# Optimization experiments

Hardware: AMD Instinct MI355X
Metric: run time of the kernel (lower is better)

Reference implementation:

```python
import jax, jax.numpy as jnp
import numpy as np

B, H, W, IMG_CH = 64, 16, 16, 1024
N, TEXT_CH = 256, 768
FQ = FK = 512


def _glorot(key, shape, fan_in, fan_out):
    lim = np.sqrt(6.0 / (fan_in + fan_out)).astype(np.float32)
    return jax.random.uniform(key, shape, jnp.float32, -lim, lim)


def setup_inputs() -> dict:
    key = jax.random.key(0)
    ks = jax.random.split(key, 8)
    x1 = jax.random.normal(ks[0], (B, H, W, IMG_CH), jnp.float32)
    x2 = jax.random.normal(ks[1], (B, N, TEXT_CH), jnp.float32)
    # padding mask over text tokens, broadcast over image pixels
    masks = (jax.random.uniform(ks[2], (B, N, 1)) > 0.1).astype(jnp.float32)
    kernel_q = _glorot(ks[3], (1, 1, IMG_CH, FQ), IMG_CH, FQ)
    kernel_k = _glorot(ks[4], (1, TEXT_CH, FK), TEXT_CH, FK)
    kernel_v = _glorot(ks[5], (1, TEXT_CH, IMG_CH), TEXT_CH, IMG_CH)
    kernel_o = _glorot(ks[6], (1, 1, IMG_CH, IMG_CH), IMG_CH, IMG_CH)
    return {
        "x1": x1, "x2": x2, "masks": masks,
        "kernel_q": kernel_q, "bias_q": jnp.zeros((FQ,), jnp.float32),
        "kernel_k": kernel_k, "bias_k": jnp.zeros((FK,), jnp.float32),
        "kernel_v": kernel_v, "bias_v": jnp.zeros((IMG_CH,), jnp.float32),
        "kernel_o": kernel_o, "bias_o": jnp.zeros((IMG_CH,), jnp.float32),
    }


def reference(x1, x2, masks, kernel_q, bias_q, kernel_k, bias_k,
              kernel_v, bias_v, kernel_o, bias_o):
    b, h, w, c = x1.shape
    # 1x1 conv2d == pointwise matmul over channels
    q = jnp.einsum('bhwc,cf->bhwf', x1, kernel_q[0, 0]) + bias_q   # (B,H,W,512)
    # width-1 conv1d == pointwise matmul over channels
    k = jnp.einsum('bnc,cf->bnf', x2, kernel_k[0]) + bias_k        # (B,N,512)
    v = jnp.einsum('bnc,cf->bnf', x2, kernel_v[0]) + bias_v        # (B,N,IMG_CH)
    qf = q.reshape(b, h * w, -1)                                   # (B,HW,512)
    s = jnp.einsum('bqd,bnd->bqn', qf, k)                          # (B,HW,N)
    beta = jax.nn.softmax(s, axis=-1)
    # NON-STANDARD: mask applied AFTER softmax (no renormalization)
    beta = beta * jnp.swapaxes(masks, 1, 2)                        # (B,HW,N)*(B,1,N)
    o = jnp.einsum('bqn,bnf->bqf', beta, v).reshape(b, h, w, c)    # (B,H,W,IMG_CH)
    o = jnp.einsum('bhwc,cf->bhwf', o, kernel_o[0, 0]) + bias_o
    return o, beta
```

## Files before the change

### kernel.cpp

```cpp
#include <hip/hip_runtime.h>
#include <hip/hip_bf16.h>

using bf16 = __hip_bfloat16;

typedef __attribute__((ext_vector_type(8))) short short8;
typedef __attribute__((ext_vector_type(4))) short shortx4;
typedef __attribute__((ext_vector_type(4))) float f32x4;

#define MFMA_BF16(a, b, c) __builtin_amdgcn_mfma_f32_16x16x32_bf16((a), (b), (c), 0, 0, 0)

__device__ __forceinline__ void lds_load16(const void* g, void* l) {
    __builtin_amdgcn_global_load_lds(
        (const __attribute__((address_space(1))) void*)g,
        (__attribute__((address_space(3))) void*)l, 16, 0, 0);
}

__device__ __forceinline__ void swiz_xcd(int& bx, int& by) {
    const int NX = gridDim.x, NY = gridDim.y;
    const int flat = blockIdx.y * NX + blockIdx.x;
    const int cid = flat & 7, slot = flat >> 3;
    by = cid * (NY >> 3) + slot / NX;
    bx = slot % NX;
}

__device__ __forceinline__ void stage_async_128(const bf16* src, int ld, bf16* tile,
                                                int wave, int lane) {
    const int r = lane >> 2, c = (lane & 3) * 8;
#pragma unroll
    for (int p = 0; p < 2; ++p) {
        const int row = p * 64 + wave * 16;
        lds_load16(src + (size_t)(row + r) * ld + c, tile + row * 32);
    }
}
__device__ __forceinline__ void stage_async_256_w8(const bf16* src, int ld, bf16* tile,
                                                   int wave, int lane) {
    const int r = lane >> 2, c = (lane & 3) * 8;
#pragma unroll
    for (int p = 0; p < 2; ++p) {
        const int row = p * 128 + wave * 16;
        lds_load16(src + (size_t)(row + r) * ld + c, tile + row * 32);
    }
}
template <bool SPLIT>
__device__ __forceinline__ void stage_conv_128(const float* src, int ld, bf16* th,
                                               bf16* tl, int tid) {
#pragma unroll
    for (int it = 0; it < 4; ++it) {
        const int vid = tid + 256 * it;
        const int row = vid >> 3, col = (vid & 7) * 4;
        const f32x4 x = *(const f32x4*)(src + (size_t)row * ld + col);
        shortx4 h, l;
#pragma unroll
        for (int j = 0; j < 4; ++j) {
            bf16 hb = __float2bfloat16(x[j]);
            h[j] = *(short*)&hb;
            if constexpr (SPLIT) {
                bf16 lb = __float2bfloat16(x[j] - __bfloat162float(hb));
                l[j] = *(short*)&lb;
            }
        }
        *(shortx4*)(&th[row * 40 + col]) = h;
        if constexpr (SPLIT) *(shortx4*)(&tl[row * 40 + col]) = l;
    }
}

template <bool SPLIT>
__global__ void transpose_split(const float* __restrict__ in, bf16* __restrict__ outh,
                                bf16* __restrict__ outl, int K, int N) {
    __shared__ float t[32][33];
    const int n0 = blockIdx.x * 32, k0 = blockIdx.y * 32;
    const int tx = threadIdx.x, ty = threadIdx.y;
#pragma unroll
    for (int i = 0; i < 4; ++i)
        t[ty + i * 8][tx] = in[(size_t)(k0 + ty + i * 8) * N + n0 + tx];
    __syncthreads();
#pragma unroll
    for (int i = 0; i < 4; ++i) {
        const float x = t[tx][ty + i * 8];
        const bf16 hb = __float2bfloat16(x);
        const size_t idx = (size_t)(n0 + ty + i * 8) * K + k0 + tx;
        outh[idx] = hb;
        if constexpr (SPLIT) outl[idx] = __float2bfloat16(x - __bfloat162float(hb));
    }
}

enum { G_SPLIT3 = 0, G_VT = 1, G_F32 = 2, G_PV = 3 };

template <int MODE>
__global__ __launch_bounds__(256) void gemm2(
    const void* __restrict__ Av, const bf16* __restrict__ Bth,
    const bf16* __restrict__ Btl, const float* __restrict__ bias,
    void* __restrict__ out0, void* __restrict__ out1, int N, int K) {
    constexpr bool ASPLIT = (MODE == G_SPLIT3);
    constexpr bool ACONV = (MODE == G_SPLIT3 || MODE == G_VT);
    constexpr int LDA = ACONV ? 40 : 32;
    constexpr int SZ_A = 128 * LDA * 2;
    constexpr int SZ_AL = ASPLIT ? 128 * 40 * 2 : 0;
    constexpr int SZ_B = 128 * 32 * 2;
    constexpr int STAGE = SZ_A + SZ_AL + SZ_B + (ASPLIT ? SZ_B : 0);
    constexpr int SMEM =
        (MODE == G_VT) ? (STAGE > 128 * 136 * 2 ? STAGE : 128 * 136 * 2) : STAGE;
    __shared__ __align__(16) char smem[SMEM];
    bf16* AsH = (bf16*)smem;
    bf16* AsL = (bf16*)(smem + SZ_A);
    bf16* BsH = (bf16*)(smem + SZ_A + SZ_AL);
    bf16* BsL = (bf16*)(smem + SZ_A + SZ_AL + SZ_B);
    bf16* Ts = (bf16*)smem;

    const int tid = threadIdx.x, wave = tid >> 6, lane = tid & 63;
    const int quad = lane >> 4, l15 = lane & 15;
    const int wr = wave >> 1, wc = wave & 1;

    int bx, by;
    if constexpr (MODE == G_PV) {
        bx = blockIdx.x;
        by = blockIdx.y;
    } else {
        swiz_xcd(bx, by);
    }
    const int m0 = by * 128, n0 = bx * 128;
    const int z = blockIdx.z;

    const float* Af = (const float*)Av;
    const bf16* Ab = (const bf16*)Av;
    const bf16* Bh = Bth;
    if constexpr (MODE == G_PV) {
        Ab += (size_t)z * 256 * 256;
        Bh += (size_t)z * 1024 * 256;
    }

    f32x4 acc[4][4] = {};
    for (int k0 = 0; k0 < K; k0 += 32) {
        if constexpr (ACONV)
            stage_conv_128<ASPLIT>(Af + (size_t)m0 * K + k0, K, AsH, AsL, tid);
        else
            stage_async_128(Ab + (size_t)m0 * K + k0, K, AsH, wave, lane);
        stage_async_128(Bh + (size_t)n0 * K + k0, K, BsH, wave, lane);
        if constexpr (ASPLIT)
            stage_async_128(Btl + (size_t)n0 * K + k0, K, BsL, wave, lane);
        __syncthreads();

        short8 ah[4], bh[4];
#pragma unroll
        for (int t = 0; t < 4; ++t) {
            ah[t] = *(const short8*)(&AsH[(wr * 64 + t * 16 + l15) * LDA + quad * 8]);
            bh[t] = *(const short8*)(&BsH[(wc * 64 + t * 16 + l15) * 32 + quad * 8]);
        }
        if constexpr (ASPLIT) {
            short8 al[4], bl[4];
#pragma unroll
            for (int t = 0; t < 4; ++t) {
                al[t] = *(const short8*)(&AsL[(wr * 64 + t * 16 + l15) * 40 + quad * 8]);
                bl[t] = *(const short8*)(&BsL[(wc * 64 + t * 16 + l15) * 32 + quad * 8]);
            }
#pragma unroll
            for (int ti = 0; ti < 4; ++ti)
#pragma unroll
                for (int tj = 0; tj < 4; ++tj) {
                    acc[ti][tj] = MFMA_BF16(al[ti], bh[tj], acc[ti][tj]);
                    acc[ti][tj] = MFMA_BF16(ah[ti], bl[tj], acc[ti][tj]);
                    acc[ti][tj] = MFMA_BF16(ah[ti], bh[tj], acc[ti][tj]);
                }
        } else {
#pragma unroll
            for (int ti = 0; ti < 4; ++ti)
#pragma unroll
                for (int tj = 0; tj < 4; ++tj)
                    acc[ti][tj] = MFMA_BF16(ah[ti], bh[tj], acc[ti][tj]);
        }
        __syncthreads();
    }

    float bv4[4] = {0.f, 0.f, 0.f, 0.f};
    if constexpr (MODE != G_PV) {
#pragma unroll
        for (int tj = 0; tj < 4; ++tj) bv4[tj] = bias[n0 + wc * 64 + tj * 16 + l15];
    }

    if constexpr (MODE == G_VT) {
#pragma unroll
        for (int ti = 0; ti < 4; ++ti)
#pragma unroll
            for (int tj = 0; tj < 4; ++tj)
#pragma unroll
                for (int i = 0; i < 4; ++i) {
                    const int ml = wr * 64 + ti * 16 + quad * 4 + i;
                    const int nl = wc * 64 + tj * 16 + l15;
                    Ts[nl * 136 + ml] = __float2bfloat16(acc[ti][tj][i] + bv4[tj]);
                }
        __syncthreads();
        const int bIdx = m0 >> 8, tok0 = m0 & 255;
        const int nl = tid >> 1, half = tid & 1;
        bf16* dst = (bf16*)out0 + ((size_t)bIdx * N + n0 + nl) * 256 + tok0 + half * 64;
        const bf16* src = &Ts[nl * 136 + half * 64];
#pragma unroll
        for (int j = 0; j < 8; ++j)
            *(short8*)(dst + j * 8) = *(const short8*)(src + j * 8);
    } else {
#pragma unroll
        for (int ti = 0; ti < 4; ++ti)
#pragma unroll
            for (int tj = 0; tj < 4; ++tj)
#pragma unroll
                for (int i = 0; i < 4; ++i) {
                    const size_t row = m0 + wr * 64 + ti * 16 + quad * 4 + i;
                    const size_t col = n0 + wc * 64 + tj * 16 + l15;
                    const float v = acc[ti][tj][i] + bv4[tj];
                    if constexpr (MODE == G_F32) {
                        ((float*)out0)[row * N + col] = v;
                    } else if constexpr (MODE == G_PV) {
                        ((bf16*)out0)[((size_t)z * 256 + row) * N + col] =
                            __float2bfloat16(v);
                    } else {
                        const bf16 hb = __float2bfloat16(v);
                        ((bf16*)out0)[row * N + col] = hb;
                        ((bf16*)out1)[row * N + col] =
                            __float2bfloat16(v - __bfloat162float(hb));
                    }
                }
    }
}

__global__ __launch_bounds__(512) void attn_s(
    const bf16* __restrict__ qh, const bf16* __restrict__ ql,
    const bf16* __restrict__ kh, const bf16* __restrict__ kl,
    const float* __restrict__ masks, float* __restrict__ beta_out,
    bf16* __restrict__ betaB) {
    __shared__ bf16 kH[256 * 32], kL[256 * 32];
    __shared__ float redM[4][32], redS[4][32];
    int qt, b;
    swiz_xcd(qt, b);
    const int tid = threadIdx.x, wave = tid >> 6, lane = tid & 63;
    const int quad = lane >> 4, l15 = lane & 15;
    const int wr = wave >> 2, wq = wave & 3;

    f32x4 acc[4] = {};
    const size_t qoff = ((size_t)(b * 256 + qt * 32 + wr * 16 + l15)) * 512;
    const size_t kbase = (size_t)(b * 256) * 512;

    for (int k0 = 0; k0 < 512; k0 += 32) {
        stage_async_256_w8(kh + kbase + k0, 512, kH, wave, lane);
        stage_async_256_w8(kl + kbase + k0, 512, kL, wave, lane);
        __syncthreads();
        const short8 aH = *(const short8*)(qh + qoff + k0 + quad * 8);
        const short8 aL = *(const short8*)(ql + qoff + k0 + quad * 8);
#pragma unroll
        for (int nt = 0; nt < 4; ++nt) {
            const int kr = wq * 64 + nt * 16 + l15;
            const short8 bH = *(const short8*)(&kH[kr * 32 + quad * 8]);
            const short8 bL = *(const short8*)(&kL[kr * 32 + quad * 8]);
            acc[nt] = MFMA_BF16(aH, bH, acc[nt]);
            acc[nt] = MFMA_BF16(aH, bL, acc[nt]);
            acc[nt] = MFMA_BF16(aL, bH, acc[nt]);
        }
        __syncthreads();
    }

    float pm[4], ps[4];
#pragma unroll
    for (int i = 0; i < 4; ++i) {
        float m = fmaxf(fmaxf(acc[0][i], acc[1][i]), fmaxf(acc[2][i], acc[3][i]));
#pragma unroll
        for (int s = 1; s < 16; s <<= 1) m = fmaxf(m, __shfl_xor(m, s));
        float sum = 0.f;
#pragma unroll
        for (int nt = 0; nt < 4; ++nt) sum += __expf(acc[nt][i] - m);
#pragma unroll
        for (int s = 1; s < 16; s <<= 1) sum += __shfl_xor(sum, s);
        pm[i] = m;
        ps[i] = sum;
    }
    if (l15 == 0) {
#pragma unroll
        for (int i = 0; i < 4; ++i) {
            redM[wq][wr * 16 + quad * 4 + i] = pm[i];
            redS[wq][wr * 16 + quad * 4 + i] = ps[i];
        }
    }
    __syncthreads();
    float gm[4], ginv[4];
#pragma unroll
    for (int i = 0; i < 4; ++i) {
        const int r = wr * 16 + quad * 4 + i;
        const float m = fmaxf(fmaxf(redM[0][r], redM[1][r]), fmaxf(redM[2][r], redM[3][r]));
        const float s = redS[0][r] * __expf(redM[0][r] - m) +
                        redS[1][r] * __expf(redM[1][r] - m) +
                        redS[2][r] * __expf(redM[2][r] - m) +
                        redS[3][r] * __expf(redM[3][r] - m);
        gm[i] = m;
        ginv[i] = 1.0f / s;
    }
#pragma unroll
    for (int nt = 0; nt < 4; ++nt) {
        const int col = wq * 64 + nt * 16 + l15;
        const float mv = masks[b * 256 + col];
#pragma unroll
        for (int i = 0; i < 4; ++i) {
            const int row = qt * 32 + wr * 16 + quad * 4 + i;
            const float bvv = __expf(acc[nt][i] - gm[i]) * ginv[i] * mv;
            const size_t idx = ((size_t)(b * 256 + row)) * 256 + col;
            beta_out[idx] = bvv;
            betaB[idx] = __float2bfloat16(bvv);
        }
    }
}

extern "C" void kernel_launch(void* const* d_in, const int* in_sizes, int n_in,
                              void* d_out, int out_size, void* d_ws, size_t ws_size,
                              hipStream_t stream) {
    const float* x1 = (const float*)d_in[0];
    const float* x2 = (const float*)d_in[1];
    const float* masks = (const float*)d_in[2];
    const float* Wq = (const float*)d_in[3];
    const float* bq = (const float*)d_in[4];
    const float* Wk = (const float*)d_in[5];
    const float* bk = (const float*)d_in[6];
    const float* Wv = (const float*)d_in[7];
    const float* bv = (const float*)d_in[8];
    const float* Wo = (const float*)d_in[9];
    const float* bo = (const float*)d_in[10];

    char* ws = (char*)d_ws;
    bf16* WqTh = (bf16*)(ws + 0);
    bf16* WqTl = (bf16*)(ws + 1048576);
    bf16* WkTh = (bf16*)(ws + 2097152);
    bf16* WkTl = (bf16*)(ws + 2883584);
    bf16* WvTh = (bf16*)(ws + 3670016);
    bf16* WoTh = (bf16*)(ws + 5242880);
    bf16* qh = (bf16*)(ws + 7340032);
    bf16* ql = (bf16*)(ws + 24117248);
    bf16* kh = (bf16*)(ws + 40894464);
    bf16* kl = (bf16*)(ws + 57671680);
    bf16* vT = (bf16*)(ws + 74448896);
    bf16* betaB = (bf16*)(ws + 108003328);
    bf16* o_mid = (bf16*)(ws + 7340032);

    float* out_o = (float*)d_out;
    float* out_beta = out_o + (size_t)16384 * 1024;

    const dim3 tb(32, 8);
    transpose_split<true><<<dim3(16, 32), tb, 0, stream>>>(Wq, WqTh, WqTl, 1024, 512);
    transpose_split<true><<<dim3(16, 24), tb, 0, stream>>>(Wk, WkTh, WkTl, 768, 512);
    transpose_split<false><<<dim3(32, 24), tb, 0, stream>>>(Wv, WvTh, nullptr, 768, 1024);
    transpose_split<false><<<dim3(32, 32), tb, 0, stream>>>(Wo, WoTh, nullptr, 1024, 1024);

    gemm2<G_SPLIT3><<<dim3(4, 128), 256, 0, stream>>>(x1, WqTh, WqTl, bq, qh, ql, 512, 1024);
    gemm2<G_SPLIT3><<<dim3(4, 128), 256, 0, stream>>>(x2, WkTh, WkTl, bk, kh, kl, 512, 768);
    gemm2<G_VT><<<dim3(8, 128), 256, 0, stream>>>(x2, WvTh, nullptr, bv, vT, nullptr, 1024, 768);

    attn_s<<<dim3(8, 64), 512, 0, stream>>>(qh, ql, kh, kl, masks, out_beta, betaB);

    gemm2<G_PV><<<dim3(8, 2, 64), 256, 0, stream>>>(betaB, vT, nullptr, nullptr, o_mid,
                                                    nullptr, 1024, 256);
    gemm2<G_F32><<<dim3(8, 128), 256, 0, stream>>>(o_mid, WoTh, nullptr, bo, out_o,
                                                   nullptr, 1024, 1024);
}
```

Measured before the change: 472.3 us.

## Stage fp32 A tiles via async LDS loads and XOR-swizzle LDS tiles

The A operand of the converting GEMMs is no longer loaded into registers, split into bf16 hi/lo and written to padded LDS. It is now copied raw as fp32 into LDS with async global_load_lds, and the bf16 hi/lo split happens at fragment-read time. All bf16 and fp32 LDS tiles also get an XOR swizzle on the 16-byte column chunk to avoid bank conflicts without padding. This removes the synchronous conversion stage and its register round trip. In exchange, each wave repeats the conversion for the fragments it reads, and the fp32 A tile takes more LDS.

```diff
diff --git a/kernel.cpp b/kernel.cpp
--- a/kernel.cpp
+++ b/kernel.cpp
@@ -23,44 +23,56 @@
     bx = slot % NX;
 }
 
-__device__ __forceinline__ void stage_async_128(const bf16* src, int ld, bf16* tile,
-                                                int wave, int lane) {
-    const int r = lane >> 2, c = (lane & 3) * 8;
+__device__ __forceinline__ void stage_bf16_128(const bf16* src, int ld, bf16* tile,
+                                               int wave, int lane) {
+    const int r = lane >> 2;
+    const int c = ((lane & 3) ^ ((r >> 1) & 3)) * 8;
 #pragma unroll
     for (int p = 0; p < 2; ++p) {
         const int row = p * 64 + wave * 16;
         lds_load16(src + (size_t)(row + r) * ld + c, tile + row * 32);
     }
 }
-__device__ __forceinline__ void stage_async_256_w8(const bf16* src, int ld, bf16* tile,
-                                                   int wave, int lane) {
-    const int r = lane >> 2, c = (lane & 3) * 8;
+__device__ __forceinline__ void stage_bf16_256_w8(const bf16* src, int ld, bf16* tile,
+                                                  int wave, int lane) {
+    const int r = lane >> 2;
+    const int c = ((lane & 3) ^ ((r >> 1) & 3)) * 8;
 #pragma unroll
     for (int p = 0; p < 2; ++p) {
         const int row = p * 128 + wave * 16;
         lds_load16(src + (size_t)(row + r) * ld + c, tile + row * 32);
     }
 }
+__device__ __forceinline__ void stage_f32_128(const float* src, int ld, float* tile,
+                                              int wave, int lane) {
+    const int r = lane >> 3;
+    const int c = ((lane & 7) ^ r) * 4;
+#pragma unroll
+    for (int it = 0; it < 4; ++it) {
+        const int row = it * 32 + wave * 8;
+        lds_load16(src + (size_t)(row + r) * ld + c, tile + row * 32);
+    }
+}
+
+__device__ __forceinline__ short8 rd_bf16(const bf16* tile, int row, int quad) {
+    const int c = (quad ^ ((row >> 1) & 3)) * 8;
+    return *(const short8*)(tile + row * 32 + c);
+}
 template <bool SPLIT>
-__device__ __forceinline__ void stage_conv_128(const float* src, int ld, bf16* th,
-                                               bf16* tl, int tid) {
-#pragma unroll
-    for (int it = 0; it < 4; ++it) {
-        const int vid = tid + 256 * it;
-        const int row = vid >> 3, col = (vid & 7) * 4;
-        const f32x4 x = *(const f32x4*)(src + (size_t)row * ld + col);
-        shortx4 h, l;
-#pragma unroll
-        for (int j = 0; j < 4; ++j) {
-            bf16 hb = __float2bfloat16(x[j]);
-            h[j] = *(short*)&hb;
-            if constexpr (SPLIT) {
-                bf16 lb = __float2bfloat16(x[j] - __bfloat162float(hb));
-                l[j] = *(short*)&lb;
-            }
-        }
-        *(shortx4*)(&th[row * 40 + col]) = h;
-        if constexpr (SPLIT) *(shortx4*)(&tl[row * 40 + col]) = l;
+__device__ __forceinline__ void rd_f32_hilo(const float* tile, int row, int quad,
+                                            short8& h, short8& l) {
+    const int f = row & 7;
+    const f32x4 x0 = *(const f32x4*)(tile + row * 32 + ((2 * quad) ^ f) * 4);
+    const f32x4 x1 = *(const f32x4*)(tile + row * 32 + ((2 * quad + 1) ^ f) * 4);
+    float xs[8] = {x0[0], x0[1], x0[2], x0[3], x1[0], x1[1], x1[2], x1[3]};
+#pragma unroll
+    for (int j = 0; j < 8; ++j) {
+        const bf16 hb = __float2bfloat16(xs[j]);
+        h[j] = *(const short*)&hb;
+        if constexpr (SPLIT) {
+            const bf16 lb = __float2bfloat16(xs[j] - __bfloat162float(hb));
+            l[j] = *(const short*)&lb;
+        }
     }
 }
 
@@ -93,18 +105,16 @@
     void* __restrict__ out0, void* __restrict__ out1, int N, int K) {
     constexpr bool ASPLIT = (MODE == G_SPLIT3);
     constexpr bool ACONV = (MODE == G_SPLIT3 || MODE == G_VT);
-    constexpr int LDA = ACONV ? 40 : 32;
-    constexpr int SZ_A = 128 * LDA * 2;
-    constexpr int SZ_AL = ASPLIT ? 128 * 40 * 2 : 0;
+    constexpr int SZ_A = ACONV ? 128 * 32 * 4 : 128 * 32 * 2;
     constexpr int SZ_B = 128 * 32 * 2;
-    constexpr int STAGE = SZ_A + SZ_AL + SZ_B + (ASPLIT ? SZ_B : 0);
+    constexpr int STAGE = SZ_A + SZ_B + (ASPLIT ? SZ_B : 0);
     constexpr int SMEM =
         (MODE == G_VT) ? (STAGE > 128 * 136 * 2 ? STAGE : 128 * 136 * 2) : STAGE;
     __shared__ __align__(16) char smem[SMEM];
+    float* AsF = (float*)smem;
     bf16* AsH = (bf16*)smem;
-    bf16* AsL = (bf16*)(smem + SZ_A);
-    bf16* BsH = (bf16*)(smem + SZ_A + SZ_AL);
-    bf16* BsL = (bf16*)(smem + SZ_A + SZ_AL + SZ_B);
+    bf16* BsH = (bf16*)(smem + SZ_A);
+    bf16* BsL = (bf16*)(smem + SZ_A + SZ_B);
     bf16* Ts = (bf16*)smem;
 
     const int tid = threadIdx.x, wave = tid >> 6, lane = tid & 63;
@@ -132,27 +142,27 @@
     f32x4 acc[4][4] = {};
     for (int k0 = 0; k0 < K; k0 += 32) {
         if constexpr (ACONV)
-            stage_conv_128<ASPLIT>(Af + (size_t)m0 * K + k0, K, AsH, AsL, tid);
+            stage_f32_128(Af + (size_t)m0 * K + k0, K, AsF, wave, lane);
         else
-            stage_async_128(Ab + (size_t)m0 * K + k0, K, AsH, wave, lane);
-        stage_async_128(Bh + (size_t)n0 * K + k0, K, BsH, wave, lane);
+            stage_bf16_128(Ab + (size_t)m0 * K + k0, K, AsH, wave, lane);
+        stage_bf16_128(Bh + (size_t)n0 * K + k0, K, BsH, wave, lane);
         if constexpr (ASPLIT)
-            stage_async_128(Btl + (size_t)n0 * K + k0, K, BsL, wave, lane);
-        __syncthreads();
-
-        short8 ah[4], bh[4];
+            stage_bf16_128(Btl + (size_t)n0 * K + k0, K, BsL, wave, lane);
+        __syncthreads();
+
+        short8 ah[4], al[4], bh[4], bl[4];
 #pragma unroll
         for (int t = 0; t < 4; ++t) {
-            ah[t] = *(const short8*)(&AsH[(wr * 64 + t * 16 + l15) * LDA + quad * 8]);
-            bh[t] = *(const short8*)(&BsH[(wc * 64 + t * 16 + l15) * 32 + quad * 8]);
+            const int ra = wr * 64 + t * 16 + l15;
+            const int rb = wc * 64 + t * 16 + l15;
+            if constexpr (ACONV)
+                rd_f32_hilo<ASPLIT>(AsF, ra, quad, ah[t], al[t]);
+            else
+                ah[t] = rd_bf16(AsH, ra, quad);
+            bh[t] = rd_bf16(BsH, rb, quad);
+            if constexpr (ASPLIT) bl[t] = rd_bf16(BsL, rb, quad);
         }
         if constexpr (ASPLIT) {
-            short8 al[4], bl[4];
-#pragma unroll
-            for (int t = 0; t < 4; ++t) {
-                al[t] = *(const short8*)(&AsL[(wr * 64 + t * 16 + l15) * 40 + quad * 8]);
-                bl[t] = *(const short8*)(&BsL[(wc * 64 + t * 16 + l15) * 32 + quad * 8]);
-            }
 #pragma unroll
             for (int ti = 0; ti < 4; ++ti)
 #pragma unroll
@@ -239,16 +249,16 @@
     const size_t kbase = (size_t)(b * 256) * 512;
 
     for (int k0 = 0; k0 < 512; k0 += 32) {
-        stage_async_256_w8(kh + kbase + k0, 512, kH, wave, lane);
-        stage_async_256_w8(kl + kbase + k0, 512, kL, wave, lane);
+        stage_bf16_256_w8(kh + kbase + k0, 512, kH, wave, lane);
+        stage_bf16_256_w8(kl + kbase + k0, 512, kL, wave, lane);
         __syncthreads();
         const short8 aH = *(const short8*)(qh + qoff + k0 + quad * 8);
         const short8 aL = *(const short8*)(ql + qoff + k0 + quad * 8);
 #pragma unroll
         for (int nt = 0; nt < 4; ++nt) {
             const int kr = wq * 64 + nt * 16 + l15;
-            const short8 bH = *(const short8*)(&kH[kr * 32 + quad * 8]);
-            const short8 bL = *(const short8*)(&kL[kr * 32 + quad * 8]);
+            const short8 bH = rd_bf16(kH, kr, quad);
+            const short8 bL = rd_bf16(kL, kr, quad);
             acc[nt] = MFMA_BF16(aH, bH, acc[nt]);
             acc[nt] = MFMA_BF16(aH, bL, acc[nt]);
             acc[nt] = MFMA_BF16(aL, bH, acc[nt]);
```

Result: faster. 444.4 us (-5.9%).
